# Kernel optimization log

Measured on AMD Instinct MI355X. Metric: run time of the kernel, lower is better.

The kernel has to match this reference:

```python
import jax, jax.numpy as jnp
import numpy as np

N, E, IN, HID, H, L, CLS = 10000, 160000, 512, 128, 8, 4, 2
ALPHA = 0.1  # residual weight
BN_EPS = 1e-5
NEG_SLOPE = 0.2  # PyG GATConv leaky_relu default


def setup_inputs() -> dict:
    key = jax.random.key(0)
    ks = jax.random.split(key, 16)
    s = 0.05
    return {
        "x": jax.random.normal(ks[0], (N, IN), jnp.float32),
        "edge_index": jax.random.randint(ks[1], (2, E), 0, N, jnp.int64),
        "Wp": jax.random.normal(ks[2], (IN, HID), jnp.float32) * s,
        "bp": jax.random.normal(ks[3], (HID,), jnp.float32) * s,
        # stacked per-layer GATConv params (shared src/dst weight as in PyG)
        "Wl": jax.random.normal(ks[4], (L, HID, H * HID), jnp.float32) * s,
        "att_src": jax.random.normal(ks[5], (L, H, HID), jnp.float32) * s,
        "att_dst": jax.random.normal(ks[6], (L, H, HID), jnp.float32) * s,
        "bl": jax.random.normal(ks[7], (L, HID), jnp.float32) * s,
        # BatchNorm (eval mode: running_mean=0, running_var=1)
        "gamma": 1.0 + jax.random.normal(ks[8], (L, HID), jnp.float32) * s,
        "beta": jax.random.normal(ks[9], (L, HID), jnp.float32) * s,
        # classifier
        "W1": jax.random.normal(ks[10], (HID, HID // 2), jnp.float32) * s,
        "b1": jax.random.normal(ks[11], (HID // 2,), jnp.float32) * s,
        "W2": jax.random.normal(ks[12], (HID // 2, CLS), jnp.float32) * s,
        "b2": jax.random.normal(ks[13], (CLS,), jnp.float32) * s,
    }


def gat_layer(h, src, dst, W, a_src, a_dst, bias):
    # h: [N, HID]; W: [HID, H*HID]
    xl = (h @ W).reshape(N, H, HID)                 # [N, H, C]
    alpha_s = jnp.sum(xl * a_src[None], axis=-1)     # [N, H]
    alpha_d = jnp.sum(xl * a_dst[None], axis=-1)     # [N, H]
    e = jax.nn.leaky_relu(alpha_s[src] + alpha_d[dst], NEG_SLOPE)  # [E', H]
    # segment softmax over incoming edges of each dst node
    emax = jax.ops.segment_max(e, dst, num_segments=N)
    ee = jnp.exp(e - emax[dst])
    denom = jax.ops.segment_sum(ee, dst, num_segments=N)
    att = ee / (denom[dst] + 1e-16)                  # [E', H]
    msg = xl[src] * att[:, :, None]                  # [E', H, C]
    out = jax.ops.segment_sum(msg, dst, num_segments=N)  # [N, H, C]
    return out.mean(axis=1) + bias                   # concat=False -> mean over heads


def reference(x, edge_index, Wp, bp, Wl, att_src, att_dst, bl, gamma, beta, W1, b1, W2, b2):
    # add self-loops (PyG GATConv default add_self_loops=True)
    loop = jnp.arange(N, dtype=edge_index.dtype)
    src = jnp.concatenate([edge_index[0], loop])
    dst = jnp.concatenate([edge_index[1], loop])

    h = jax.nn.elu(x @ Wp + bp)
    bn_inv = 1.0 / jnp.sqrt(1.0 + BN_EPS)
    for i in range(L):
        prev = h
        g = gat_layer(h, src, dst, Wl[i], att_src[i], att_dst[i], bl[i])
        g = gamma[i] * (g * bn_inv) + beta[i]        # BN eval (mean 0, var 1)
        h = jax.nn.elu((1.0 - ALPHA) * g + ALPHA * prev)
        # dropout is identity in eval mode
    hid = jax.nn.elu(h @ W1 + b1)
    return hid @ W2 + b2                             # [N, CLS]
```

## Files before the change

kernel.cpp:

```cpp
#include <hip/hip_runtime.h>
#include <cstdint>
#include <cstddef>

#define N_NODES 10000
#define N_EDGES 160000
#define DIM_IN  512
#define HIDDIM  128
#define NHEAD   8
#define NLAYER  4

typedef unsigned int   uint32;
typedef unsigned short ushort16;
typedef __attribute__((ext_vector_type(8))) short bf16x8;
typedef __attribute__((ext_vector_type(4))) float f32x4;

static __device__ __forceinline__ float eluf(float v)  { return v > 0.f ? v : expm1f(v); }
static __device__ __forceinline__ float lrelu(float v) { return v >= 0.f ? v : 0.2f * v; }
static __device__ __forceinline__ ushort16 f2bf(float f) {
    uint32 u = __float_as_uint(f);
    u += 0x7fffu + ((u >> 16) & 1u);
    return (ushort16)(u >> 16);
}
static __device__ __forceinline__ float blo(uint32 u) { return __uint_as_float(u << 16); }
static __device__ __forceinline__ float bhi(uint32 u) { return __uint_as_float(u & 0xffff0000u); }

#define BN_INV 0.9999950000374997f

__global__ void k_deg(const int* __restrict__ ei, int* __restrict__ deg) {
    int t = blockIdx.x * 256 + threadIdx.x;
    if (t < N_EDGES) atomicAdd(&deg[ei[N_EDGES + t]], 1);
}

__global__ __launch_bounds__(1024) void k_scan(const int* __restrict__ deg,
                                               int* __restrict__ rowptr,
                                               int* __restrict__ cursor) {
    __shared__ int sd[1024];
    __shared__ int carry;
    int tid = threadIdx.x;
    if (tid == 0) { carry = 0; rowptr[0] = 0; }
    __syncthreads();
    for (int base = 0; base < N_NODES; base += 1024) {
        int i = base + tid;
        int v = (i < N_NODES) ? (deg[i] + 1) : 0;
        sd[tid] = v;
        __syncthreads();
        for (int ofs = 1; ofs < 1024; ofs <<= 1) {
            int t = (tid >= ofs) ? sd[tid - ofs] : 0;
            __syncthreads();
            sd[tid] += t;
            __syncthreads();
        }
        int inc = sd[tid] + carry;
        if (i < N_NODES) { rowptr[i + 1] = inc; cursor[i] = inc - v; }
        __syncthreads();
        if (tid == 1023) carry = inc;
        __syncthreads();
    }
}

__global__ void k_scatter(const int* __restrict__ ei, int* __restrict__ cursor,
                          int* __restrict__ csr) {
    int t = blockIdx.x * 256 + threadIdx.x;
    if (t < N_EDGES) {
        int s = ei[t];
        int d = ei[N_EDGES + t];
        int p = atomicAdd(&cursor[d], 1);
        csr[p] = s;
    } else if (t < N_EDGES + N_NODES) {
        int n = t - N_EDGES;
        int p = atomicAdd(&cursor[n], 1);
        csr[p] = n;
    }
}

template <int NB, int ACT, int OUTBF>
__global__ __launch_bounds__(256) void k_gemm_mfma(const float* __restrict__ A,
                                                   const float* __restrict__ B,
                                                   const float* __restrict__ bias,
                                                   void* __restrict__ Cv,
                                                   int M, int Nn, int K) {
    __shared__ unsigned short BsU[NB * 16 * 128];
    char* BsB = (char*)BsU;
    const int tid = threadIdx.x;
    const int lane = tid & 63;
    const int wv = tid >> 6;
    const int row0 = blockIdx.y * 64, col0 = blockIdx.x * (NB * 16);
    const int r = lane & 15, q = lane >> 4;

    const int arow = row0 + wv * 16 + r;
    const bool rowok = arow < M;
    const float* Ap = A + (size_t)arow * K;

    f32x4 acc[NB];
#pragma unroll
    for (int i = 0; i < NB; i++) acc[i] = (f32x4){0.f, 0.f, 0.f, 0.f};

    for (int k0 = 0; k0 < K; k0 += 128) {
        __syncthreads();
#pragma unroll
        for (int it = 0; it < NB * 2; it++) {
            int gq = tid + it * 256;
            int kk = gq / (NB * 4);
            int c4 = (gq % (NB * 4)) * 4;
            float4 v = *(const float4*)(B + (size_t)(k0 + kk) * Nn + col0 + c4);
            float vv[4] = {v.x, v.y, v.z, v.w};
#pragma unroll
            for (int c = 0; c < 4; c++) {
                int col = c4 + c;
                int byte = (col * 256 + kk * 2) ^ ((col & 7) << 4);
                *(unsigned short*)(BsB + byte) = f2bf(vv[c]);
            }
        }
        __syncthreads();
#pragma unroll
        for (int ks = 0; ks < 4; ks++) {
            int ka = k0 + ks * 32 + q * 8;
            float4 a0 = make_float4(0.f, 0.f, 0.f, 0.f);
            float4 a1 = make_float4(0.f, 0.f, 0.f, 0.f);
            if (rowok) {
                a0 = *(const float4*)(Ap + ka);
                a1 = *(const float4*)(Ap + ka + 4);
            }
            bf16x8 af;
            af[0] = (short)f2bf(a0.x); af[1] = (short)f2bf(a0.y);
            af[2] = (short)f2bf(a0.z); af[3] = (short)f2bf(a0.w);
            af[4] = (short)f2bf(a1.x); af[5] = (short)f2bf(a1.y);
            af[6] = (short)f2bf(a1.z); af[7] = (short)f2bf(a1.w);
            int kb = (ks * 32 + q * 8) * 2;
#pragma unroll
            for (int nb = 0; nb < NB; nb++) {
                int col = nb * 16 + r;
                bf16x8 bfr = *(bf16x8*)(BsB + ((col * 256 + kb) ^ ((col & 7) << 4)));
                acc[nb] = __builtin_amdgcn_mfma_f32_16x16x32_bf16(af, bfr, acc[nb], 0, 0, 0);
            }
        }
    }
#pragma unroll
    for (int nb = 0; nb < NB; nb++) {
        int col = col0 + nb * 16 + r;
#pragma unroll
        for (int j = 0; j < 4; j++) {
            int row = row0 + wv * 16 + q * 4 + j;
            if (row < M) {
                float v = acc[nb][j];
                if (ACT) { v += bias[col]; v = eluf(v); }
                if (OUTBF) ((unsigned short*)Cv)[(size_t)row * Nn + col] = f2bf(v);
                else       ((float*)Cv)[(size_t)row * Nn + col] = v;
            }
        }
    }
}

__global__ __launch_bounds__(256) void k_alphas(const ushort16* __restrict__ xl,
                                                const float* __restrict__ atts,
                                                const float* __restrict__ attd,
                                                float* __restrict__ as_,
                                                float* __restrict__ ad_) {
    int lane = threadIdx.x & 63;
    int n = blockIdx.x * 4 + (threadIdx.x >> 6);
    if (n >= N_NODES) return;
    int g = lane >> 4;
    int c8 = 8 * (lane & 15);
    const uint4* xp = (const uint4*)(xl + (size_t)n * 1024);
    float ss[2], sd[2];
#pragma unroll
    for (int j = 0; j < 2; j++) {
        int head = 4 * j + g;
        uint4 u = xp[j * 64 + lane];
        const float4* ap = (const float4*)(atts + head * 128 + c8);
        const float4* bp = (const float4*)(attd + head * 128 + c8);
        float4 a0 = ap[0], a1 = ap[1];
        float4 b0 = bp[0], b1 = bp[1];
        float x0 = blo(u.x), x1 = bhi(u.x), x2 = blo(u.y), x3 = bhi(u.y);
        float x4 = blo(u.z), x5 = bhi(u.z), x6 = blo(u.w), x7 = bhi(u.w);
        ss[j] = x0 * a0.x + x1 * a0.y + x2 * a0.z + x3 * a0.w +
                x4 * a1.x + x5 * a1.y + x6 * a1.z + x7 * a1.w;
        sd[j] = x0 * b0.x + x1 * b0.y + x2 * b0.z + x3 * b0.w +
                x4 * b1.x + x5 * b1.y + x6 * b1.z + x7 * b1.w;
    }
#pragma unroll
    for (int m = 1; m < 16; m <<= 1) {
#pragma unroll
        for (int j = 0; j < 2; j++) {
            ss[j] += __shfl_xor(ss[j], m);
            sd[j] += __shfl_xor(sd[j], m);
        }
    }
    if ((lane & 15) == 0) {
        as_[n * 8 + g]     = ss[0];
        as_[n * 8 + 4 + g] = ss[1];
        ad_[n * 8 + g]     = sd[0];
        ad_[n * 8 + 4 + g] = sd[1];
    }
}

__global__ __launch_bounds__(256) void k_aggregate(const int* __restrict__ rowptr,
                                                   const int* __restrict__ csr,
                                                   const float* __restrict__ as_,
                                                   const float* __restrict__ ad_,
                                                   const ushort16* __restrict__ xl,
                                                   const float* __restrict__ hprev,
                                                   const float* __restrict__ bl,
                                                   const float* __restrict__ gam,
                                                   const float* __restrict__ bet,
                                                   float* __restrict__ hnext) {
    __shared__ float cmb[2][64][17];
    int tid = threadIdx.x;
    int lane = tid & 63;
    int wv = tid >> 6;
    int which = wv >> 1;
    int par = wv & 1;
    int n = blockIdx.x * 2 + which;
    int h8 = lane & 7;
    int g = lane >> 4;
    float adh = ad_[n * 8 + h8];
    int start = rowptr[n], end = rowptr[n + 1];

    float acc0[8] = {}, acc1[8] = {};
    float denom = 0.f;
    int e = start + par;
    for (; e + 2 < end; e += 4) {
        int s0 = csr[e], s1 = csr[e + 2];
        float a0 = as_[s0 * 8 + h8];
        float a1 = as_[s1 * 8 + h8];
        const uint4* xp0 = (const uint4*)(xl + (size_t)s0 * 1024);
        const uint4* xp1 = (const uint4*)(xl + (size_t)s1 * 1024);
        uint4 u0a = xp0[lane], u1a = xp0[64 + lane];
        uint4 u0b = xp1[lane], u1b = xp1[64 + lane];
        float ee0 = __expf(lrelu(a0 + adh));
        float ee1 = __expf(lrelu(a1 + adh));
        denom += ee0 + ee1;
        float e0a = __shfl(ee0, g), e1a = __shfl(ee0, 4 + g);
        float e0b = __shfl(ee1, g), e1b = __shfl(ee1, 4 + g);
        acc0[0] += e0a * blo(u0a.x) + e0b * blo(u0b.x);
        acc0[1] += e0a * bhi(u0a.x) + e0b * bhi(u0b.x);
        acc0[2] += e0a * blo(u0a.y) + e0b * blo(u0b.y);
        acc0[3] += e0a * bhi(u0a.y) + e0b * bhi(u0b.y);
        acc0[4] += e0a * blo(u0a.z) + e0b * blo(u0b.z);
        acc0[5] += e0a * bhi(u0a.z) + e0b * bhi(u0b.z);
        acc0[6] += e0a * blo(u0a.w) + e0b * blo(u0b.w);
        acc0[7] += e0a * bhi(u0a.w) + e0b * bhi(u0b.w);
        acc1[0] += e1a * blo(u1a.x) + e1b * blo(u1b.x);
        acc1[1] += e1a * bhi(u1a.x) + e1b * bhi(u1b.x);
        acc1[2] += e1a * blo(u1a.y) + e1b * blo(u1b.y);
        acc1[3] += e1a * bhi(u1a.y) + e1b * bhi(u1b.y);
        acc1[4] += e1a * blo(u1a.z) + e1b * blo(u1b.z);
        acc1[5] += e1a * bhi(u1a.z) + e1b * bhi(u1b.z);
        acc1[6] += e1a * blo(u1a.w) + e1b * blo(u1b.w);
        acc1[7] += e1a * bhi(u1a.w) + e1b * bhi(u1b.w);
    }
    for (; e < end; e += 2) {
        int s0 = csr[e];
        float a0 = as_[s0 * 8 + h8];
        const uint4* xp0 = (const uint4*)(xl + (size_t)s0 * 1024);
        uint4 u0a = xp0[lane], u1a = xp0[64 + lane];
        float ee0 = __expf(lrelu(a0 + adh));
        denom += ee0;
        float e0a = __shfl(ee0, g), e1a = __shfl(ee0, 4 + g);
        acc0[0] += e0a * blo(u0a.x); acc0[1] += e0a * bhi(u0a.x);
        acc0[2] += e0a * blo(u0a.y); acc0[3] += e0a * bhi(u0a.y);
        acc0[4] += e0a * blo(u0a.z); acc0[5] += e0a * bhi(u0a.z);
        acc0[6] += e0a * blo(u0a.w); acc0[7] += e0a * bhi(u0a.w);
        acc1[0] += e1a * blo(u1a.x); acc1[1] += e1a * bhi(u1a.x);
        acc1[2] += e1a * blo(u1a.y); acc1[3] += e1a * bhi(u1a.y);
        acc1[4] += e1a * blo(u1a.z); acc1[5] += e1a * bhi(u1a.z);
        acc1[6] += e1a * blo(u1a.w); acc1[7] += e1a * bhi(u1a.w);
    }

    if (par == 1) {
#pragma unroll
        for (int i = 0; i < 8; i++) {
            cmb[which][lane][i]     = acc0[i];
            cmb[which][lane][8 + i] = acc1[i];
        }
        cmb[which][lane][16] = denom;
    }
    __syncthreads();
    if (par == 1) return;
#pragma unroll
    for (int i = 0; i < 8; i++) {
        acc0[i] += cmb[which][lane][i];
        acc1[i] += cmb[which][lane][8 + i];
    }
    denom += cmb[which][lane][16];

    float d0 = __shfl(denom, g);
    float d1 = __shfl(denom, 4 + g);
    float r0 = 1.f / (d0 + 1e-16f);
    float r1 = 1.f / (d1 + 1e-16f);
    float sum[8];
#pragma unroll
    for (int i = 0; i < 8; i++) sum[i] = acc0[i] * r0 + acc1[i] * r1;
#pragma unroll
    for (int i = 0; i < 8; i++) {
        sum[i] += __shfl_xor(sum[i], 16);
        sum[i] += __shfl_xor(sum[i], 32);
    }

    if (lane < 16) {
        int c = 8 * lane;
        float o[8];
#pragma unroll
        for (int t = 0; t < 8; t++) {
            float m = sum[t] * 0.125f + bl[c + t];
            float gg = gam[c + t] * (m * BN_INV) + bet[c + t];
            float z = 0.9f * gg + 0.1f * hprev[(size_t)n * 128 + c + t];
            o[t] = eluf(z);
        }
        *(float4*)(hnext + (size_t)n * 128 + c)     = make_float4(o[0], o[1], o[2], o[3]);
        *(float4*)(hnext + (size_t)n * 128 + c + 4) = make_float4(o[4], o[5], o[6], o[7]);
    }
}

__global__ __launch_bounds__(256) void k_classifier(const float* __restrict__ h,
                                                    const float* __restrict__ W1,
                                                    const float* __restrict__ b1,
                                                    const float* __restrict__ W2,
                                                    const float* __restrict__ b2,
                                                    float* __restrict__ out) {
    __shared__ float sW1[128 * 64];
    __shared__ float sW2[128];
    __shared__ float sb1[64];
    __shared__ float sb2[2];
    for (int i = threadIdx.x; i < 2048; i += 256)
        *(float4*)&sW1[i * 4] = *(const float4*)(W1 + i * 4);
    if (threadIdx.x < 64) sb1[threadIdx.x] = b1[threadIdx.x];
    if (threadIdx.x < 128) sW2[threadIdx.x] = W2[threadIdx.x];
    if (threadIdx.x < 2) sb2[threadIdx.x] = b2[threadIdx.x];
    __syncthreads();
    int lane = threadIdx.x & 63;
    int n = blockIdx.x * 4 + (threadIdx.x >> 6);
    if (n >= N_NODES) return;
    float h0 = h[(size_t)n * 128 + lane];
    float h1 = h[(size_t)n * 128 + 64 + lane];
    float acc = sb1[lane];
#pragma unroll
    for (int c = 0; c < 64; c++) acc += __shfl(h0, c) * sW1[c * 64 + lane];
#pragma unroll
    for (int c = 0; c < 64; c++) acc += __shfl(h1, c) * sW1[(64 + c) * 64 + lane];
    acc = eluf(acc);
    float p0 = acc * sW2[lane * 2 + 0];
    float p1 = acc * sW2[lane * 2 + 1];
#pragma unroll
    for (int m = 1; m < 64; m <<= 1) {
        p0 += __shfl_xor(p0, m);
        p1 += __shfl_xor(p1, m);
    }
    if (lane == 0) {
        out[(size_t)n * 2 + 0] = p0 + sb2[0];
        out[(size_t)n * 2 + 1] = p1 + sb2[1];
    }
}

extern "C" void kernel_launch(void* const* d_in, const int* in_sizes, int n_in,
                              void* d_out, int out_size, void* d_ws, size_t ws_size,
                              hipStream_t stream) {
    const float* x       = (const float*)d_in[0];
    const int* ei        = (const int*)d_in[1];
    const float* Wp      = (const float*)d_in[2];
    const float* bp      = (const float*)d_in[3];
    const float* Wl      = (const float*)d_in[4];
    const float* atts    = (const float*)d_in[5];
    const float* attd    = (const float*)d_in[6];
    const float* bl      = (const float*)d_in[7];
    const float* gam     = (const float*)d_in[8];
    const float* bet     = (const float*)d_in[9];
    const float* W1      = (const float*)d_in[10];
    const float* b1      = (const float*)d_in[11];
    const float* W2      = (const float*)d_in[12];
    const float* b2      = (const float*)d_in[13];
    float* out = (float*)d_out;

    char* w = (char*)d_ws;
    auto carve = [&](size_t bytes) -> void* {
        void* p = (void*)w;
        w += (bytes + 255) & ~(size_t)255;
        return p;
    };
    int* deg        = (int*)carve((size_t)N_NODES * 4);
    int* rowptr     = (int*)carve((size_t)(N_NODES + 1) * 4);
    int* cursor     = (int*)carve((size_t)N_NODES * 4);
    int* csr        = (int*)carve((size_t)(N_EDGES + N_NODES) * 4);
    float* as_      = (float*)carve((size_t)N_NODES * 8 * 4);
    float* ad_      = (float*)carve((size_t)N_NODES * 8 * 4);
    ushort16* xl    = (ushort16*)carve((size_t)N_NODES * 1024 * 2);
    float* hA       = (float*)carve((size_t)N_NODES * 128 * 4);
    float* hB       = (float*)carve((size_t)N_NODES * 128 * 4);

    hipMemsetAsync(deg, 0, (size_t)N_NODES * 4, stream);
    k_deg<<<(N_EDGES + 255) / 256, 256, 0, stream>>>(ei, deg);
    k_scan<<<1, 1024, 0, stream>>>(deg, rowptr, cursor);
    k_scatter<<<(N_EDGES + N_NODES + 255) / 256, 256, 0, stream>>>(ei, cursor, csr);

    k_gemm_mfma<8, 1, 0><<<dim3(1, 157), 256, 0, stream>>>(x, Wp, bp, hA, N_NODES, 128, 512);

    float* hc = hA;
    float* hn = hB;
    for (int l = 0; l < NLAYER; l++) {
        k_gemm_mfma<16, 0, 1><<<dim3(4, 157), 256, 0, stream>>>(hc, Wl + (size_t)l * 128 * 1024,
                                                                nullptr, xl, N_NODES, 1024, 128);
        k_alphas<<<2500, 256, 0, stream>>>(xl, atts + l * 1024, attd + l * 1024, as_, ad_);
        k_aggregate<<<5000, 256, 0, stream>>>(rowptr, csr, as_, ad_, xl, hc, bl + l * 128,
                                              gam + l * 128, bet + l * 128, hn);
        float* tmp = hc; hc = hn; hn = tmp;
    }
    k_classifier<<<2500, 256, 0, stream>>>(hc, W1, b1, W2, b2, out);
}
```

Baseline: 595.7 us.

## Pre-transpose weights to bf16 and read B fragments directly from global

Adds a transpose kernel that converts each weight matrix once per call into a column-major bf16 copy. The GEMM then loads B fragments straight from global/L2 instead of staging them through LDS, which drops the per-block fp32-to-bf16 conversion, the LDS writes and both syncthreads. The layer GEMM also moves from 16 to 8 column blocks per workgroup, doubling the grid. The cost is five extra small kernel launches, and B fragments are now reread from cache by every wave with less reuse.

```diff
diff --git a/kernel.cpp b/kernel.cpp
--- a/kernel.cpp
+++ b/kernel.cpp
@@ -73,14 +73,33 @@
     }
 }
 
+__global__ __launch_bounds__(256) void k_transB(const float* __restrict__ B,
+                                                unsigned short* __restrict__ Wt,
+                                                int K, int Nn) {
+    __shared__ unsigned short t[32][33];
+    int bx = blockIdx.x * 32;
+    int by = blockIdx.y * 32;
+    int tx = threadIdx.x & 31;
+    int ty4 = (threadIdx.x >> 5) * 4;
+#pragma unroll
+    for (int i = 0; i < 4; i++) {
+        int k = by + ty4 + i;
+        t[ty4 + i][tx] = f2bf(B[(size_t)k * Nn + bx + tx]);
+    }
+    __syncthreads();
+#pragma unroll
+    for (int i = 0; i < 4; i++) {
+        int col = bx + ty4 + i;
+        Wt[(size_t)col * K + by + tx] = t[tx][ty4 + i];
+    }
+}
+
 template <int NB, int ACT, int OUTBF>
-__global__ __launch_bounds__(256) void k_gemm_mfma(const float* __restrict__ A,
-                                                   const float* __restrict__ B,
-                                                   const float* __restrict__ bias,
-                                                   void* __restrict__ Cv,
-                                                   int M, int Nn, int K) {
-    __shared__ unsigned short BsU[NB * 16 * 128];
-    char* BsB = (char*)BsU;
+__global__ __launch_bounds__(256) void k_gemm_dmfma(const float* __restrict__ A,
+                                                    const unsigned short* __restrict__ Wt,
+                                                    const float* __restrict__ bias,
+                                                    void* __restrict__ Cv,
+                                                    int M, int Nn, int K) {
     const int tid = threadIdx.x;
     const int lane = tid & 63;
     const int wv = tid >> 6;
@@ -95,44 +114,25 @@
 #pragma unroll
     for (int i = 0; i < NB; i++) acc[i] = (f32x4){0.f, 0.f, 0.f, 0.f};
 
-    for (int k0 = 0; k0 < K; k0 += 128) {
-        __syncthreads();
-#pragma unroll
-        for (int it = 0; it < NB * 2; it++) {
-            int gq = tid + it * 256;
-            int kk = gq / (NB * 4);
-            int c4 = (gq % (NB * 4)) * 4;
-            float4 v = *(const float4*)(B + (size_t)(k0 + kk) * Nn + col0 + c4);
-            float vv[4] = {v.x, v.y, v.z, v.w};
-#pragma unroll
-            for (int c = 0; c < 4; c++) {
-                int col = c4 + c;
-                int byte = (col * 256 + kk * 2) ^ ((col & 7) << 4);
-                *(unsigned short*)(BsB + byte) = f2bf(vv[c]);
-            }
-        }
-        __syncthreads();
-#pragma unroll
-        for (int ks = 0; ks < 4; ks++) {
-            int ka = k0 + ks * 32 + q * 8;
-            float4 a0 = make_float4(0.f, 0.f, 0.f, 0.f);
-            float4 a1 = make_float4(0.f, 0.f, 0.f, 0.f);
-            if (rowok) {
-                a0 = *(const float4*)(Ap + ka);
-                a1 = *(const float4*)(Ap + ka + 4);
-            }
-            bf16x8 af;
-            af[0] = (short)f2bf(a0.x); af[1] = (short)f2bf(a0.y);
-            af[2] = (short)f2bf(a0.z); af[3] = (short)f2bf(a0.w);
-            af[4] = (short)f2bf(a1.x); af[5] = (short)f2bf(a1.y);
-            af[6] = (short)f2bf(a1.z); af[7] = (short)f2bf(a1.w);
-            int kb = (ks * 32 + q * 8) * 2;
-#pragma unroll
-            for (int nb = 0; nb < NB; nb++) {
-                int col = nb * 16 + r;
-                bf16x8 bfr = *(bf16x8*)(BsB + ((col * 256 + kb) ^ ((col & 7) << 4)));
-                acc[nb] = __builtin_amdgcn_mfma_f32_16x16x32_bf16(af, bfr, acc[nb], 0, 0, 0);
-            }
+    const int nks = K >> 5;
+    for (int ks = 0; ks < nks; ks++) {
+        int ko = ks * 32 + q * 8;
+        float4 a0 = make_float4(0.f, 0.f, 0.f, 0.f);
+        float4 a1 = make_float4(0.f, 0.f, 0.f, 0.f);
+        if (rowok) {
+            a0 = *(const float4*)(Ap + ko);
+            a1 = *(const float4*)(Ap + ko + 4);
+        }
+        bf16x8 af;
+        af[0] = (short)f2bf(a0.x); af[1] = (short)f2bf(a0.y);
+        af[2] = (short)f2bf(a0.z); af[3] = (short)f2bf(a0.w);
+        af[4] = (short)f2bf(a1.x); af[5] = (short)f2bf(a1.y);
+        af[6] = (short)f2bf(a1.z); af[7] = (short)f2bf(a1.w);
+#pragma unroll
+        for (int nb = 0; nb < NB; nb++) {
+            int col = col0 + nb * 16 + r;
+            bf16x8 bfr = *(const bf16x8*)(Wt + (size_t)col * K + ko);
+            acc[nb] = __builtin_amdgcn_mfma_f32_16x16x32_bf16(af, bfr, acc[nb], 0, 0, 0);
         }
     }
 #pragma unroll
@@ -386,19 +386,26 @@
     ushort16* xl    = (ushort16*)carve((size_t)N_NODES * 1024 * 2);
     float* hA       = (float*)carve((size_t)N_NODES * 128 * 4);
     float* hB       = (float*)carve((size_t)N_NODES * 128 * 4);
+    unsigned short* WtP = (unsigned short*)carve((size_t)128 * 512 * 2);
+    unsigned short* WtL = (unsigned short*)carve((size_t)NLAYER * 1024 * 128 * 2);
 
     hipMemsetAsync(deg, 0, (size_t)N_NODES * 4, stream);
     k_deg<<<(N_EDGES + 255) / 256, 256, 0, stream>>>(ei, deg);
     k_scan<<<1, 1024, 0, stream>>>(deg, rowptr, cursor);
     k_scatter<<<(N_EDGES + N_NODES + 255) / 256, 256, 0, stream>>>(ei, cursor, csr);
 
-    k_gemm_mfma<8, 1, 0><<<dim3(1, 157), 256, 0, stream>>>(x, Wp, bp, hA, N_NODES, 128, 512);
+    k_transB<<<dim3(4, 16), 256, 0, stream>>>(Wp, WtP, 512, 128);
+    for (int l = 0; l < NLAYER; l++)
+        k_transB<<<dim3(32, 4), 256, 0, stream>>>(Wl + (size_t)l * 128 * 1024,
+                                                  WtL + (size_t)l * 1024 * 128, 128, 1024);
+
+    k_gemm_dmfma<8, 1, 0><<<dim3(1, 157), 256, 0, stream>>>(x, WtP, bp, hA, N_NODES, 128, 512);
 
     float* hc = hA;
     float* hn = hB;
     for (int l = 0; l < NLAYER; l++) {
-        k_gemm_mfma<16, 0, 1><<<dim3(4, 157), 256, 0, stream>>>(hc, Wl + (size_t)l * 128 * 1024,
-                                                                nullptr, xl, N_NODES, 1024, 128);
+        k_gemm_dmfma<8, 0, 1><<<dim3(8, 157), 256, 0, stream>>>(
+            hc, WtL + (size_t)l * 1024 * 128, nullptr, xl, N_NODES, 1024, 128);
         k_alphas<<<2500, 256, 0, stream>>>(xl, atts + l * 1024, attd + l * 1024, as_, ad_);
         k_aggregate<<<5000, 256, 0, stream>>>(rowptr, csr, as_, ad_, xl, hc, bl + l * 128,
                                               gam + l * 128, bet + l * 128, hn);
```

After: 516.5 us. 13.3% less time.
